# Optimization experiments

Measured on AMD Instinct MI355X. Metric: run time of the kernel, lower is better.

Reference implementation:

```python
import jax, jax.numpy as jnp
import numpy as np

B, N, C, H = 4, 2048, 1024, 16
D = C // H  # head_dim


def setup_inputs() -> dict:
    key = jax.random.key(0)
    ks = jax.random.split(key, 9)
    s = 1.0 / np.sqrt(C)
    return {
        "x": jax.random.normal(ks[0], (B, N, C), dtype=jnp.float32),
        "Wq": jax.random.uniform(ks[1], (C, C), jnp.float32, -s, s),
        "bq": jax.random.uniform(ks[2], (C,), jnp.float32, -s, s),
        "Wk": jax.random.uniform(ks[3], (C, C), jnp.float32, -s, s),
        "bk": jax.random.uniform(ks[4], (C,), jnp.float32, -s, s),
        "Wv": jax.random.uniform(ks[5], (C, C), jnp.float32, -s, s),
        "bv": jax.random.uniform(ks[6], (C,), jnp.float32, -s, s),
        "Wo": jax.random.uniform(ks[7], (C, C), jnp.float32, -s, s),
        "bo": jax.random.uniform(ks[8], (C,), jnp.float32, -s, s),
    }


def reference(x, Wq, bq, Wk, bk, Wv, bv, Wo, bo):
    # QKV projections -> [B, H, N, D]
    def proj(W, b):
        y = jnp.einsum('bnc,cd->bnd', x, W) + b
        return y.reshape(B, N, H, D).transpose(0, 2, 1, 3)

    q = proj(Wq, bq)
    k = proj(Wk, bk)
    v = proj(Wv, bv)

    scale = 1.0 / np.sqrt(D).astype(np.float32)
    scores = jnp.einsum('bhnd,bhmd->bhnm', q, k) * scale  # [B,H,N,N]
    probs = jax.nn.softmax(scores, axis=-1)
    out = jnp.einsum('bhnm,bhmd->bhnd', probs, v)  # [B,H,N,D]
    out = out.transpose(0, 2, 1, 3).reshape(B, N, C)
    return jnp.einsum('bnc,cd->bnd', out, Wo) + bo
```

## Files before the change

### kernel.cpp

```cpp
#include <hip/hip_runtime.h>
#include <hip/hip_bf16.h>
#include <stdint.h>


#define DEV __device__ __forceinline__

typedef unsigned short u16;
typedef __attribute__((ext_vector_type(8))) _Float16 f16x8;
typedef __attribute__((ext_vector_type(4))) float f32x4;

DEV u16 f2h(float f) {
    _Float16 h = (_Float16)f;
    return __builtin_bit_cast(u16, h);
}

DEV unsigned int pk2h(float a, float b) {
    return __builtin_bit_cast(unsigned int, __builtin_amdgcn_cvt_pkrtz(a, b));
}

#define GLD16(gp, lp)                                                         \
    __builtin_amdgcn_global_load_lds(                                         \
        (__attribute__((address_space(1))) void*)(gp),                        \
        (__attribute__((address_space(3))) void*)(lp), 16, 0, 0)

DEV f32x4 mfma16(f16x8 a, f16x8 b, f32x4 c) {
    return __builtin_amdgcn_mfma_f32_16x16x32_f16(a, b, c, 0, 0, 0);
}

__global__ void cast_fuse(const float* __restrict__ x,
                          const float* __restrict__ Wq, const float* __restrict__ Wk,
                          const float* __restrict__ Wv, const float* __restrict__ Wo,
                          u16* __restrict__ xb, u16* __restrict__ Wt4) {
    __shared__ float lds[64 * 68];
    int bid = blockIdx.x, tid = threadIdx.x;
    if (bid < 4096) {
        size_t base = (size_t)bid * 2048 + (size_t)tid * 8;
        float4 v0 = *(const float4*)(x + base);
        float4 v1 = *(const float4*)(x + base + 4);
        union { u16 u[8]; uint4 v; } p;
        p.u[0] = f2h(v0.x); p.u[1] = f2h(v0.y); p.u[2] = f2h(v0.z); p.u[3] = f2h(v0.w);
        p.u[4] = f2h(v1.x); p.u[5] = f2h(v1.y); p.u[6] = f2h(v1.z); p.u[7] = f2h(v1.w);
        *(uint4*)(xb + base) = p.v;
        return;
    }
    bid -= 4096;
    int wsel = bid >> 8, t = bid & 255;
    int k0 = (t >> 4) * 64, n0 = (t & 15) * 64;
    const float* W = wsel == 0 ? Wq : wsel == 1 ? Wk : wsel == 2 ? Wv : Wo;
    u16* Wt = Wt4 + (size_t)wsel * 1048576;
#pragma unroll
    for (int i = 0; i < 4; i++) {
        int slot = tid * 4 + i * 1024;
        int rr = slot >> 6, cc = slot & 63;
        float4 v = *(const float4*)(W + (size_t)(k0 + rr) * 1024 + n0 + cc);
        *(float4*)(&lds[rr * 68 + cc]) = v;
    }
    __syncthreads();
    int n = tid >> 2, kc = (tid & 3) * 16;
    union { u16 u[16]; uint4 v[2]; } p;
#pragma unroll
    for (int j = 0; j < 16; j++) p.u[j] = f2h(lds[(kc + j) * 68 + n]);
    u16* dst = Wt + (size_t)(n0 + n) * 1024 + k0 + kc;
    *(uint4*)(dst) = p.v[0];
    *(uint4*)(dst + 8) = p.v[1];
}

DEV void gemm_core(const u16* __restrict__ A, const u16* __restrict__ Wt,
                   int m0, int n0, f32x4 (&acc)[4][4]) {
    __shared__ u16 Alds[2][128 * 32];
    __shared__ u16 Blds[2][128 * 32];
    const int tid = threadIdx.x, lane = tid & 63;
    const int w = tid >> 6, g = lane >> 4, r16 = lane & 15;
    const int wm = (w >> 1) * 64, wn = (w & 1) * 64;
#pragma unroll
    for (int i = 0; i < 4; i++)
#pragma unroll
        for (int j = 0; j < 4; j++) acc[i][j] = f32x4{0.f, 0.f, 0.f, 0.f};

    auto stage = [&](int buf, int kt) {
        int k0 = kt * 64;
#pragma unroll
        for (int i = 0; i < 2; i++) {
            int slot = i * 4096 + tid * 16;
            int rr = slot >> 6, cc = slot & 63;
            GLD16((const char*)A + (size_t)(m0 + rr) * 2048 + k0 + cc,
                  (char*)Alds[buf] + slot);
            GLD16((const char*)Wt + (size_t)(n0 + rr) * 2048 + k0 + cc,
                  (char*)Blds[buf] + slot);
        }
    };
    stage(0, 0);
    __syncthreads();

    for (int kt = 0; kt < 32; ++kt) {
        int cur = kt & 1;
        if (kt < 31) stage(cur ^ 1, kt + 1);
        f16x8 af[4], bf[4];
#pragma unroll
        for (int i = 0; i < 4; i++) {
            af[i] = *(const f16x8*)((const char*)Alds[cur] + (wm + i * 16 + r16) * 64 + g * 16);
            bf[i] = *(const f16x8*)((const char*)Blds[cur] + (wn + i * 16 + r16) * 64 + g * 16);
        }
#pragma unroll
        for (int i = 0; i < 4; i++)
#pragma unroll
            for (int j = 0; j < 4; j++) acc[i][j] = mfma16(af[i], bf[j], acc[i][j]);
        __syncthreads();
    }
}

__global__ __launch_bounds__(256, 2) void gemm_qkv(
    const u16* __restrict__ xb, const u16* __restrict__ Wt4,
    const float* __restrict__ bq, const float* __restrict__ bk,
    const float* __restrict__ bv,
    u16* __restrict__ Qo, u16* __restrict__ Ko, u16* __restrict__ Vo) {
    int m0 = blockIdx.x * 128, n0 = blockIdx.y * 128, z = blockIdx.z;
    const u16* Wt = Wt4 + (size_t)z * 1048576;
    const float* bias = z == 0 ? bq : z == 1 ? bk : bv;
    u16* Out = z == 0 ? Qo : z == 1 ? Ko : Vo;
    const float sc = (z == 0) ? 0.125f * 1.44269504f : 1.0f;
    f32x4 acc[4][4];
    gemm_core(xb, Wt, m0, n0, acc);

    __shared__ u16 Clds[128 * 136];
    const int tid = threadIdx.x, lane = tid & 63, w = tid >> 6;
    const int g = lane >> 4, r16 = lane & 15;
    const int wm = (w >> 1) * 64, wn = (w & 1) * 64;
#pragma unroll
    for (int j = 0; j < 4; j++) {
        int nl = wn + j * 16 + r16;
        float bb = bias[n0 + nl];
#pragma unroll
        for (int i = 0; i < 4; i++)
#pragma unroll
            for (int rr = 0; rr < 4; rr++) {
                int ml = wm + i * 16 + g * 4 + rr;
                Clds[ml * 136 + nl] = f2h((acc[i][j][rr] + bb) * sc);
            }
    }
    __syncthreads();
    const int b = m0 >> 11, nst = m0 & 2047;
#pragma unroll
    for (int s = 0; s < 2; s++) {
        int h = (n0 + s * 64) >> 6;
        u16* obase = Out + (((size_t)(b * 16 + h)) * 2048 + nst) * 64;
#pragma unroll
        for (int p = 0; p < 4; p++) {
            int idx = p * 256 + tid;
            int r = idx >> 3, c8 = (idx & 7) * 8;
            uint4 v = *(const uint4*)(&Clds[r * 136 + s * 64 + c8]);
            *(uint4*)(obase + (size_t)r * 64 + c8) = v;
        }
    }
}

__global__ __launch_bounds__(256, 2) void gemm_out(
    const u16* __restrict__ AO, const u16* __restrict__ Wt,
    const float* __restrict__ bo, float* __restrict__ Out) {
    int m0 = blockIdx.x * 128, n0 = blockIdx.y * 128;
    f32x4 acc[4][4];
    gemm_core(AO, Wt, m0, n0, acc);
    const int lane = threadIdx.x & 63, w = threadIdx.x >> 6;
    const int g = lane >> 4, r16 = lane & 15;
    const int wm = (w >> 1) * 64, wn = (w & 1) * 64;
#pragma unroll
    for (int j = 0; j < 4; j++) {
        int c = n0 + wn + j * 16 + r16;
        float bb = bo[c];
#pragma unroll
        for (int i = 0; i < 4; i++) {
#pragma unroll
            for (int rr = 0; rr < 4; rr++) {
                int m = m0 + wm + i * 16 + g * 4 + rr;
                Out[(size_t)m * 1024 + c] = acc[i][j][rr] + bb;
            }
        }
    }
}

__global__ void transpose_v(const u16* __restrict__ V, u16* __restrict__ VT) {
    __shared__ u16 lds[64 * 66];
    int bh = blockIdx.x >> 5, n0 = (blockIdx.x & 31) * 64;
    const u16* Vb = V + (size_t)bh * 2048 * 64;
    u16* VTb = VT + (size_t)bh * 64 * 2048;
    int tid = threadIdx.x;
#pragma unroll
    for (int i = 0; i < 8; i++) {
        int p = tid + i * 256;
        int rr = p >> 5, c2 = (p & 31) * 2;
        unsigned int val = *(const unsigned int*)(Vb + (size_t)(n0 + rr) * 64 + c2);
        *(unsigned int*)(&lds[rr * 66 + c2]) = val;
    }
    __syncthreads();
#pragma unroll
    for (int i = 0; i < 2; i++) {
        int s = tid * 8 + i * 2048;
        int d = s >> 6, ns = s & 63;
        union { u16 u[8]; uint4 v; } p;
#pragma unroll
        for (int j = 0; j < 8; j++) p.u[j] = lds[(ns + j) * 66 + d];
        *(uint4*)(VTb + (size_t)d * 2048 + n0 + ns) = p.v;
    }
}

__global__ __launch_bounds__(512, 4) void attn_k(
    const u16* __restrict__ Q, const u16* __restrict__ K,
    const u16* __restrict__ VT, u16* __restrict__ AO) {
    __shared__ char Klds[2][16384];
    __shared__ char Vlds[2][16384];
    __shared__ char Plds[8][2048];
    const int bh = blockIdx.x, q0 = blockIdx.y * 128;
    const int tid = threadIdx.x, lane = tid & 63, w = tid >> 6;
    const int g = lane >> 4, r16 = lane & 15;
    const char* Qb = (const char*)(Q + (size_t)bh * 2048 * 64);
    const char* Kb = (const char*)(K + (size_t)bh * 2048 * 64);
    const char* VTb = (const char*)(VT + (size_t)bh * 64 * 2048);
    char* Pw = Plds[w];
    const f32x4 ZZ = {0.f, 0.f, 0.f, 0.f};

    f16x8 qf[2];
#pragma unroll
    for (int ks = 0; ks < 2; ks++)
        qf[ks] = *(const f16x8*)(Qb + (size_t)(q0 + w * 16 + r16) * 128 +
                                 ks * 64 + g * 16);
    f16x8 onesf;
#pragma unroll
    for (int j = 0; j < 8; j++) onesf[j] = (_Float16)1.0f;

    f32x4 oacc[4], lacc;
#pragma unroll
    for (int dg = 0; dg < 4; dg++) oacc[dg] = ZZ;
    lacc = ZZ;

    auto stage = [&](int buf, int t) {
#pragma unroll
        for (int i = 0; i < 2; i++) {
            int slot = i * 8192 + tid * 16;
            {
                int rr = slot >> 7, cc = slot & 127;
                GLD16(Kb + (size_t)(t * 128 + rr) * 128 + (cc ^ ((rr & 7) << 4)),
                      Klds[buf] + slot);
            }
            {
                int rr = slot >> 8, cc = slot & 255;
                GLD16(VTb + (size_t)rr * 4096 + t * 256 + (cc ^ ((rr & 7) << 4)),
                      Vlds[buf] + slot);
            }
        }
    };
    stage(0, 0);
    __syncthreads();

    for (int t = 0; t < 16; ++t) {
        const int cur = t & 1;
        if (t < 15) stage(cur ^ 1, t + 1);
        const char* Kl = Klds[cur];
        const char* Vl = Vlds[cur];

        f32x4 sacc[8];
        __builtin_amdgcn_s_setprio(1);
#pragma unroll
        for (int kg = 0; kg < 8; kg++) {
            int row = kg * 16 + r16, sw = (row & 7) << 4;
            f16x8 kf0 = *(const f16x8*)(Kl + row * 128 + ((g * 16) ^ sw));
            f16x8 kf1 = *(const f16x8*)(Kl + row * 128 + ((64 + g * 16) ^ sw));
            sacc[kg] = mfma16(kf0, qf[0], ZZ);
            sacc[kg] = mfma16(kf1, qf[1], sacc[kg]);
        }
        __builtin_amdgcn_s_setprio(0);

#pragma unroll
        for (int h = 0; h < 2; h++) {
#pragma unroll
            for (int kg2 = 0; kg2 < 4; kg2++) {
                int kg = h * 4 + kg2;
                uint2 pk;
                pk.x = pk2h(exp2f(sacc[kg][0]), exp2f(sacc[kg][1]));
                pk.y = pk2h(exp2f(sacc[kg][2]), exp2f(sacc[kg][3]));
                *(uint2*)(Pw + r16 * 128 +
                          ((kg2 * 32 + g * 8) ^ ((r16 & 7) << 4))) = pk;
            }
            __builtin_amdgcn_s_setprio(1);
#pragma unroll
            for (int ks2 = 0; ks2 < 2; ks2++) {
                f16x8 pf = *(const f16x8*)(Pw + r16 * 128 +
                                           ((ks2 * 64 + g * 16) ^ ((r16 & 7) << 4)));
                f16x8 vf[4];
#pragma unroll
                for (int dg = 0; dg < 4; dg++) {
                    int row = dg * 16 + r16;
                    vf[dg] = *(const f16x8*)(Vl + row * 256 +
                                             ((h * 128 + ks2 * 64 + g * 16) ^ ((row & 7) << 4)));
                }
#pragma unroll
                for (int dg = 0; dg < 4; dg++)
                    oacc[dg] = mfma16(pf, vf[dg], oacc[dg]);
                lacc = mfma16(pf, onesf, lacc);
            }
            __builtin_amdgcn_s_setprio(0);
        }
        __syncthreads();
    }

    const int b = bh >> 4, h = bh & 15;
    float li[4];
#pragma unroll
    for (int rr = 0; rr < 4; rr++) li[rr] = 1.0f / lacc[rr];
#pragma unroll
    for (int dg = 0; dg < 4; dg++) {
        int d = dg * 16 + r16;
#pragma unroll
        for (int rr = 0; rr < 4; rr++) {
            int nrow = q0 + w * 16 + g * 4 + rr;
            AO[((size_t)(b * 2048 + nrow)) * 1024 + h * 64 + d] =
                f2h(oacc[dg][rr] * li[rr]);
        }
    }
}

extern "C" void kernel_launch(void* const* d_in, const int* in_sizes, int n_in,
                              void* d_out, int out_size, void* d_ws, size_t ws_size,
                              hipStream_t stream) {
    const float* x = (const float*)d_in[0];
    const float* Wq = (const float*)d_in[1];
    const float* bq = (const float*)d_in[2];
    const float* Wk = (const float*)d_in[3];
    const float* bk = (const float*)d_in[4];
    const float* Wv = (const float*)d_in[5];
    const float* bv = (const float*)d_in[6];
    const float* Wo = (const float*)d_in[7];
    const float* bo = (const float*)d_in[8];

    char* ws = (char*)d_ws;
    u16* xb  = (u16*)(ws);
    u16* Wt  = (u16*)(ws + (16ull << 20));
    u16* Qb  = (u16*)(ws + (24ull << 20));
    u16* Kb  = (u16*)(ws + (40ull << 20));
    u16* Vb  = (u16*)(ws + (56ull << 20));
    u16* VTb = (u16*)(ws + (72ull << 20));
    u16* AO  = (u16*)(ws + (88ull << 20));

    cast_fuse<<<dim3(5120), dim3(256), 0, stream>>>(x, Wq, Wk, Wv, Wo, xb, Wt);
    gemm_qkv<<<dim3(64, 8, 3), dim3(256), 0, stream>>>(xb, Wt, bq, bk, bv, Qb, Kb, Vb);
    transpose_v<<<dim3(2048), dim3(256), 0, stream>>>(Vb, VTb);
    attn_k<<<dim3(64, 16), dim3(512), 0, stream>>>(Qb, Kb, VTb, AO);
    gemm_out<<<dim3(64, 8), dim3(256), 0, stream>>>(AO, Wt + 3ull * 1048576, bo,
                                                    (float*)d_out);
}
```

Before: 314.3 us.

## Keep attention probabilities in registers via permuted V^T layout; drop LDS staging

The attention kernel no longer writes the exponentiated scores to a per-wave LDS buffer and reads them back. It packs them straight from the MFMA accumulators into the A-operand registers. To make this valid, transpose_v now writes V^T with a permuted key order within each 64-column block, so the accumulator layout lines up with the V operand. The QKV GEMM epilogue also drops its LDS staging and scattered-writes scalar fp16 values directly to global memory. That removes a barrier and the LDS traffic, but replaces coalesced 16-byte stores with 2-byte scattered ones.

```diff
diff --git a/kernel.cpp b/kernel.cpp
--- a/kernel.cpp
+++ b/kernel.cpp
@@ -121,35 +121,23 @@
     const float sc = (z == 0) ? 0.125f * 1.44269504f : 1.0f;
     f32x4 acc[4][4];
     gemm_core(xb, Wt, m0, n0, acc);
-
-    __shared__ u16 Clds[128 * 136];
-    const int tid = threadIdx.x, lane = tid & 63, w = tid >> 6;
+    const int lane = threadIdx.x & 63, w = threadIdx.x >> 6;
     const int g = lane >> 4, r16 = lane & 15;
     const int wm = (w >> 1) * 64, wn = (w & 1) * 64;
 #pragma unroll
     for (int j = 0; j < 4; j++) {
-        int nl = wn + j * 16 + r16;
-        float bb = bias[n0 + nl];
-#pragma unroll
-        for (int i = 0; i < 4; i++)
+        int c = n0 + wn + j * 16 + r16;
+        float bb = bias[c];
+        int h = c >> 6, d = c & 63;
+#pragma unroll
+        for (int i = 0; i < 4; i++) {
 #pragma unroll
             for (int rr = 0; rr < 4; rr++) {
-                int ml = wm + i * 16 + g * 4 + rr;
-                Clds[ml * 136 + nl] = f2h((acc[i][j][rr] + bb) * sc);
-            }
-    }
-    __syncthreads();
-    const int b = m0 >> 11, nst = m0 & 2047;
-#pragma unroll
-    for (int s = 0; s < 2; s++) {
-        int h = (n0 + s * 64) >> 6;
-        u16* obase = Out + (((size_t)(b * 16 + h)) * 2048 + nst) * 64;
-#pragma unroll
-        for (int p = 0; p < 4; p++) {
-            int idx = p * 256 + tid;
-            int r = idx >> 3, c8 = (idx & 7) * 8;
-            uint4 v = *(const uint4*)(&Clds[r * 136 + s * 64 + c8]);
-            *(uint4*)(obase + (size_t)r * 64 + c8) = v;
+                int m = m0 + wm + i * 16 + g * 4 + rr;
+                int b = m >> 11, n = m & 2047;
+                Out[(((size_t)(b * 16 + h)) * 2048 + n) * 64 + d] =
+                    f2h((acc[i][j][rr] + bb) * sc);
+            }
         }
     }
 }
@@ -196,10 +184,14 @@
     for (int i = 0; i < 2; i++) {
         int s = tid * 8 + i * 2048;
         int d = s >> 6, ns = s & 63;
-        union { u16 u[8]; uint4 v; } p;
+        union { u16 u[8]; uint2 w[2]; } p;
 #pragma unroll
         for (int j = 0; j < 8; j++) p.u[j] = lds[(ns + j) * 66 + d];
-        *(uint4*)(VTb + (size_t)d * 2048 + n0 + ns) = p.v;
+        int b0 = ns >> 2, b1 = b0 + 1;
+        int c0 = (b0 & 8) | ((b0 & 3) << 1) | ((b0 & 4) >> 2);
+        int c1 = (b1 & 8) | ((b1 & 3) << 1) | ((b1 & 4) >> 2);
+        *(uint2*)(VTb + (size_t)d * 2048 + n0 + c0 * 4) = p.w[0];
+        *(uint2*)(VTb + (size_t)d * 2048 + n0 + c1 * 4) = p.w[1];
     }
 }
 
@@ -208,14 +200,12 @@
     const u16* __restrict__ VT, u16* __restrict__ AO) {
     __shared__ char Klds[2][16384];
     __shared__ char Vlds[2][16384];
-    __shared__ char Plds[8][2048];
     const int bh = blockIdx.x, q0 = blockIdx.y * 128;
     const int tid = threadIdx.x, lane = tid & 63, w = tid >> 6;
     const int g = lane >> 4, r16 = lane & 15;
     const char* Qb = (const char*)(Q + (size_t)bh * 2048 * 64);
     const char* Kb = (const char*)(K + (size_t)bh * 2048 * 64);
     const char* VTb = (const char*)(VT + (size_t)bh * 64 * 2048);
-    char* Pw = Plds[w];
     const f32x4 ZZ = {0.f, 0.f, 0.f, 0.f};
 
     f16x8 qf[2];
@@ -272,19 +262,14 @@
 #pragma unroll
         for (int h = 0; h < 2; h++) {
 #pragma unroll
-            for (int kg2 = 0; kg2 < 4; kg2++) {
-                int kg = h * 4 + kg2;
-                uint2 pk;
-                pk.x = pk2h(exp2f(sacc[kg][0]), exp2f(sacc[kg][1]));
-                pk.y = pk2h(exp2f(sacc[kg][2]), exp2f(sacc[kg][3]));
-                *(uint2*)(Pw + r16 * 128 +
-                          ((kg2 * 32 + g * 8) ^ ((r16 & 7) << 4))) = pk;
-            }
-            __builtin_amdgcn_s_setprio(1);
-#pragma unroll
             for (int ks2 = 0; ks2 < 2; ks2++) {
-                f16x8 pf = *(const f16x8*)(Pw + r16 * 128 +
-                                           ((ks2 * 64 + g * 16) ^ ((r16 & 7) << 4)));
+                const int kg_e = h * 4 + ks2 * 2, kg_o = kg_e + 1;
+                union { unsigned u[4]; f16x8 v; } pu;
+                pu.u[0] = pk2h(exp2f(sacc[kg_e][0]), exp2f(sacc[kg_e][1]));
+                pu.u[1] = pk2h(exp2f(sacc[kg_e][2]), exp2f(sacc[kg_e][3]));
+                pu.u[2] = pk2h(exp2f(sacc[kg_o][0]), exp2f(sacc[kg_o][1]));
+                pu.u[3] = pk2h(exp2f(sacc[kg_o][2]), exp2f(sacc[kg_o][3]));
+                f16x8 pf = pu.v;
                 f16x8 vf[4];
 #pragma unroll
                 for (int dg = 0; dg < 4; dg++) {
@@ -292,12 +277,13 @@
                     vf[dg] = *(const f16x8*)(Vl + row * 256 +
                                              ((h * 128 + ks2 * 64 + g * 16) ^ ((row & 7) << 4)));
                 }
+                __builtin_amdgcn_s_setprio(1);
 #pragma unroll
                 for (int dg = 0; dg < 4; dg++)
                     oacc[dg] = mfma16(pf, vf[dg], oacc[dg]);
                 lacc = mfma16(pf, onesf, lacc);
-            }
-            __builtin_amdgcn_s_setprio(0);
+                __builtin_amdgcn_s_setprio(0);
+            }
         }
         __syncthreads();
     }
```

New measurement: 306.9 us. 2.3% less time.
